# Optimization experiments

Hardware: AMD Instinct MI355X
Metric: run time of the kernel (lower is better)

Reference implementation:

```python
import jax, jax.numpy as jnp
import numpy as np

TOP_K = 2
LORA_SCALE = 32.0 / 16.0  # alpha / rank


def setup_inputs() -> dict:
    key = jax.random.key(0)
    ks = jax.random.split(key, 11)
    N, D, F, E, R = 1024, 2048, 5632, 8, 16
    s = lambda k, shape, fan: jax.random.normal(k, shape, jnp.float32) / np.sqrt(fan)
    return {
        "x": jax.random.normal(ks[0], (N, D), jnp.float32),
        "gate_w": s(ks[1], (E, D), D),
        "W1": s(ks[2], (F, D), D),
        "W3": s(ks[3], (F, D), D),
        "W2": s(ks[4], (D, F), F),
        "A1": s(ks[5], (E, R, D), D),
        "B1": s(ks[6], (F, R), R)[None].repeat(E, 0) * 0.0 + s(ks[6], (E, F, R), R),
        "A3": s(ks[7], (E, R, D), D),
        "B3": s(ks[8], (E, F, R), R),
        "A2": s(ks[9], (E, R, F), F),
        "B2": s(ks[10], (E, D, R), R),
    }


def reference(x, gate_w, W1, W3, W2, A1, B1, A3, B3, A2, B2):
    # --- router: softmax over experts, top-k, renormalized combine weights ---
    logits = x @ gate_w.T                                   # [N, E]
    probs = jax.nn.softmax(logits, axis=-1)
    topw, topi = jax.lax.top_k(probs, TOP_K)                # [N, K]
    topw = topw / jnp.sum(topw, axis=-1, keepdims=True)
    E = gate_w.shape[0]
    w = jnp.sum(jax.nn.one_hot(topi, E, dtype=x.dtype) * topw[..., None], axis=1)  # [N, E]

    # --- experts: shared base weights + per-expert LoRA (fused SwiGLU) ---
    base1 = x @ W1.T                                        # [N, F]
    base3 = x @ W3.T                                        # [N, F]
    l1 = jnp.einsum("nd,erd->ner", x, A1)                   # rank-R bottleneck
    l3 = jnp.einsum("nd,erd->ner", x, A3)
    h1 = base1[:, None, :] + LORA_SCALE * jnp.einsum("ner,efr->nef", l1, B1)  # [N, E, F]
    h3 = base3[:, None, :] + LORA_SCALE * jnp.einsum("ner,efr->nef", l3, B3)
    s = jax.nn.silu(h1) * h3                                # [N, E, F]

    # down-projection: shared W2 applied to the routed mixture, plus per-expert LoRA
    s_mix = jnp.einsum("ne,nef->nf", w, s)                  # [N, F]
    out = s_mix @ W2.T                                      # [N, D]
    l2 = jnp.einsum("nef,erf->ner", s, A2) * (w[:, :, None] * LORA_SCALE)
    out = out + jnp.einsum("ner,edr->nd", l2, B2)           # [N, D]
    return out, logits
```

## Files before the change

### kernel.cpp

```cpp
#include <hip/hip_runtime.h>

typedef unsigned int u32;
typedef unsigned short u16;

#define N_TOK 1024
#define D_DIM 2048
#define F_DIM 5632
#define E_NUM 8
#define R_DIM 16
#define LSCALE 2.0f
#define FT 256
#define NT (F_DIM / FT)
#define TC 8
#define BN13 11520

typedef __bf16 bf16x8 __attribute__((ext_vector_type(8)));
typedef float f32x4 __attribute__((ext_vector_type(4)));
typedef u16 u16x8 __attribute__((ext_vector_type(8)));

__device__ inline u16 f2bf(float f) {
    u32 u = __builtin_bit_cast(u32, f);
    u32 r = (u + 0x7fffu + ((u >> 16) & 1u)) >> 16;
    return (u16)r;
}
__device__ inline float bf2f(u16 h) {
    u32 u = ((u32)h) << 16;
    return __builtin_bit_cast(float, u);
}

__global__ __launch_bounds__(256) void cvt_f32_bf16(const float* __restrict__ src,
                                                    u16* __restrict__ dst, int n4) {
    int i = blockIdx.x * 256 + threadIdx.x;
    if (i >= n4) return;
    float4 v = ((const float4*)src)[i];
    union { u16 h[4]; ushort4 u4; } o;
    o.h[0] = f2bf(v.x); o.h[1] = f2bf(v.y); o.h[2] = f2bf(v.z); o.h[3] = f2bf(v.w);
    ((ushort4*)dst)[i] = o.u4;
}

__global__ __launch_bounds__(256) void a2_transpose(const float* __restrict__ A2,
                                                    u16* __restrict__ A2t) {
    int e = blockIdx.y;
    int f = blockIdx.x * 256 + threadIdx.x;
    u16 row[16];
#pragma unroll
    for (int r = 0; r < 16; ++r)
        row[r] = f2bf(A2[((size_t)e * R_DIM + r) * F_DIM + f]);
    u16* dst = A2t + ((size_t)e * F_DIM + f) * 16;
#pragma unroll
    for (int q = 0; q < 2; ++q)
        ((ulonglong2*)dst)[q] = ((ulonglong2*)row)[q];
}

__global__ __launch_bounds__(256) void router_kernel(const float* __restrict__ x,
                                                     const float* __restrict__ gw,
                                                     float* __restrict__ logits,
                                                     int* __restrict__ ridx,
                                                     float* __restrict__ rw) {
    int n = blockIdx.x;
    int tid = threadIdx.x;
    float part[E_NUM];
#pragma unroll
    for (int e = 0; e < E_NUM; ++e) part[e] = 0.f;
    const float* xr = x + (size_t)n * D_DIM;
    for (int d = tid; d < D_DIM; d += 256) {
        float xv = xr[d];
#pragma unroll
        for (int e = 0; e < E_NUM; ++e) part[e] += xv * gw[e * D_DIM + d];
    }
    __shared__ float sh[E_NUM][256];
#pragma unroll
    for (int e = 0; e < E_NUM; ++e) sh[e][tid] = part[e];
    __syncthreads();
    for (int off = 128; off > 0; off >>= 1) {
        if (tid < off) {
#pragma unroll
            for (int e = 0; e < E_NUM; ++e) sh[e][tid] += sh[e][tid + off];
        }
        __syncthreads();
    }
    if (tid == 0) {
        float lg[E_NUM], p[E_NUM];
        float mx = -1e30f;
        for (int e = 0; e < E_NUM; ++e) {
            lg[e] = sh[e][0];
            logits[n * E_NUM + e] = lg[e];
            if (lg[e] > mx) mx = lg[e];
        }
        float s = 0.f;
        for (int e = 0; e < E_NUM; ++e) { p[e] = expf(lg[e] - mx); s += p[e]; }
        for (int e = 0; e < E_NUM; ++e) p[e] /= s;
        int i1 = 0;
        for (int e = 1; e < E_NUM; ++e) if (p[e] > p[i1]) i1 = e;
        int i2 = (i1 == 0) ? 1 : 0;
        for (int e = 0; e < E_NUM; ++e) if (e != i1 && p[e] > p[i2]) i2 = e;
        float t = p[i1] + p[i2];
        ridx[n * 2] = i1; ridx[n * 2 + 1] = i2;
        rw[n * 2] = p[i1] / t; rw[n * 2 + 1] = p[i2] / t;
    }
}

__global__ __launch_bounds__(64) void zero_counts(int* counts) {
    if (threadIdx.x < E_NUM) counts[threadIdx.x] = 0;
}
__global__ __launch_bounds__(256) void build_lists(const int* __restrict__ ridx,
                                                   int* __restrict__ counts,
                                                   u32* __restrict__ lists) {
    int n = blockIdx.x * 256 + threadIdx.x;
    if (n >= N_TOK) return;
#pragma unroll
    for (int k = 0; k < 2; ++k) {
        int e = ridx[n * 2 + k];
        int slot = atomicAdd(&counts[e], 1);
        lists[e * N_TOK + slot] = (u32)n | ((u32)k << 16);
    }
}

__global__ __launch_bounds__(256) void gemm_bf16_bt(const u16* __restrict__ A,
                                                    const u16* __restrict__ B,
                                                    float* __restrict__ C,
                                                    int M, int N, int K, int out_bf16) {
    __shared__ __align__(16) u16 sA[128 * 64];
    __shared__ __align__(16) u16 sB[128 * 64];
    const int tid = threadIdx.x;
    const int lane = tid & 63;
    const int wave = tid >> 6;
    const int quad = lane >> 4;
    const int l16 = lane & 15;
    const int wm = (wave & 1) * 64;
    const int wn = (wave >> 1) * 64;
    const int bm0 = blockIdx.x * 128;
    const int bn0 = blockIdx.y * 128;

    f32x4 zero = {0.f, 0.f, 0.f, 0.f};
    f32x4 acc[4][4];
#pragma unroll
    for (int i = 0; i < 4; ++i)
#pragma unroll
        for (int j = 0; j < 4; ++j) acc[i][j] = zero;

    for (int k0 = 0; k0 < K; k0 += 64) {
#pragma unroll
        for (int i = 0; i < 4; ++i) {
            int c = i * 256 + tid;
            int r = c >> 3;
            int c8 = (c & 7) << 3;
            const u16* ga = A + (size_t)(bm0 + r) * K + k0 + c8;
            const u16* gb = B + (size_t)(bn0 + r) * K + k0 + c8;
            __builtin_amdgcn_global_load_lds((const __attribute__((address_space(1))) u32*)ga,
                                             (__attribute__((address_space(3))) u32*)(sA + c * 8),
                                             16, 0, 0);
            __builtin_amdgcn_global_load_lds((const __attribute__((address_space(1))) u32*)gb,
                                             (__attribute__((address_space(3))) u32*)(sB + c * 8),
                                             16, 0, 0);
        }
        __syncthreads();
#pragma unroll
        for (int ks = 0; ks < 2; ++ks) {
            bf16x8 af[4], bfv[4];
#pragma unroll
            for (int mi = 0; mi < 4; ++mi)
                af[mi] = *(const bf16x8*)(sA + (wm + mi * 16 + l16) * 64 + ks * 32 + quad * 8);
#pragma unroll
            for (int ni = 0; ni < 4; ++ni)
                bfv[ni] = *(const bf16x8*)(sB + (wn + ni * 16 + l16) * 64 + ks * 32 + quad * 8);
#pragma unroll
            for (int mi = 0; mi < 4; ++mi)
#pragma unroll
                for (int ni = 0; ni < 4; ++ni)
                    acc[mi][ni] = __builtin_amdgcn_mfma_f32_16x16x32_bf16(af[mi], bfv[ni],
                                                                          acc[mi][ni], 0, 0, 0);
        }
        __syncthreads();
    }

#pragma unroll
    for (int mi = 0; mi < 4; ++mi)
#pragma unroll
        for (int ni = 0; ni < 4; ++ni) {
            int col = bn0 + wn + ni * 16 + l16;
#pragma unroll
            for (int i = 0; i < 4; ++i) {
                int row = bm0 + wm + mi * 16 + quad * 4 + i;
                if (out_bf16) {
                    ((u16*)C)[(size_t)row * N + col] = f2bf(acc[mi][ni][i]);
                } else {
                    C[(size_t)row * N + col] = acc[mi][ni][i];
                }
            }
        }
}

__global__ __launch_bounds__(256) void gemm_bt_splitk(const u16* __restrict__ A,
                                                      const u16* __restrict__ B,
                                                      float* __restrict__ C,
                                                      int M, int N, int K, int ksplit) {
    __shared__ __align__(16) u16 sA[128 * 64];
    __shared__ __align__(16) u16 sB[128 * 64];
    const int tid = threadIdx.x;
    const int lane = tid & 63;
    const int wave = tid >> 6;
    const int quad = lane >> 4;
    const int l16 = lane & 15;
    const int wm = (wave & 1) * 64;
    const int wn = (wave >> 1) * 64;
    const int bm0 = blockIdx.x * 128;
    const int bn0 = blockIdx.y * 128;
    const int kb = blockIdx.z * ksplit;
    const int ke = kb + ksplit;

    f32x4 zero = {0.f, 0.f, 0.f, 0.f};
    f32x4 acc[4][4];
#pragma unroll
    for (int i = 0; i < 4; ++i)
#pragma unroll
        for (int j = 0; j < 4; ++j) acc[i][j] = zero;

    for (int k0 = kb; k0 < ke; k0 += 64) {
#pragma unroll
        for (int i = 0; i < 4; ++i) {
            int c = i * 256 + tid;
            int r = c >> 3;
            int c8 = (c & 7) << 3;
            const u16* ga = A + (size_t)(bm0 + r) * K + k0 + c8;
            const u16* gb = B + (size_t)(bn0 + r) * K + k0 + c8;
            __builtin_amdgcn_global_load_lds((const __attribute__((address_space(1))) u32*)ga,
                                             (__attribute__((address_space(3))) u32*)(sA + c * 8),
                                             16, 0, 0);
            __builtin_amdgcn_global_load_lds((const __attribute__((address_space(1))) u32*)gb,
                                             (__attribute__((address_space(3))) u32*)(sB + c * 8),
                                             16, 0, 0);
        }
        __syncthreads();
#pragma unroll
        for (int ks = 0; ks < 2; ++ks) {
            bf16x8 af[4], bfv[4];
#pragma unroll
            for (int mi = 0; mi < 4; ++mi)
                af[mi] = *(const bf16x8*)(sA + (wm + mi * 16 + l16) * 64 + ks * 32 + quad * 8);
#pragma unroll
            for (int ni = 0; ni < 4; ++ni)
                bfv[ni] = *(const bf16x8*)(sB + (wn + ni * 16 + l16) * 64 + ks * 32 + quad * 8);
#pragma unroll
            for (int mi = 0; mi < 4; ++mi)
#pragma unroll
                for (int ni = 0; ni < 4; ++ni)
                    acc[mi][ni] = __builtin_amdgcn_mfma_f32_16x16x32_bf16(af[mi], bfv[ni],
                                                                          acc[mi][ni], 0, 0, 0);
        }
        __syncthreads();
    }

#pragma unroll
    for (int mi = 0; mi < 4; ++mi)
#pragma unroll
        for (int ni = 0; ni < 4; ++ni) {
            int col = bn0 + wn + ni * 16 + l16;
#pragma unroll
            for (int i = 0; i < 4; ++i) {
                int row = bm0 + wm + mi * 16 + quad * 4 + i;
                unsafeAtomicAdd(&C[(size_t)row * N + col], acc[mi][ni][i]);
            }
        }
}

__global__ __launch_bounds__(256) void act_v2b(const u16* __restrict__ base13,
                                               const u16* __restrict__ B1b,
                                               const u16* __restrict__ B3b,
                                               const u32* __restrict__ lists,
                                               const int* __restrict__ counts,
                                               const float* __restrict__ rw,
                                               u16* __restrict__ sbuf) {
    const int ft = blockIdx.x;
    const int e  = blockIdx.y;
    const int z  = blockIdx.z;
    const int tid = threadIdx.x;
    const int lane = tid & 63;
    const int wave = tid >> 6;
    const int f_lane = ft * FT + lane * 4;

    u16x8 w1c[8], w3c[8];
    {
        const u16* p1 = B1b + ((size_t)e * F_DIM + f_lane) * 16;
        const u16* p3 = B3b + ((size_t)e * F_DIM + f_lane) * 16;
#pragma unroll
        for (int c = 0; c < 8; ++c) {
            w1c[c] = *(const u16x8*)(p1 + c * 8);
            w3c[c] = *(const u16x8*)(p3 + c * 8);
        }
    }

    const int T = counts[e];
    for (int i = z * 4 + wave; i < T; i += TC * 4) {
        u32 ent = lists[e * N_TOK + i];
        int n = (int)(ent & 0xFFFFu);
        int k = (int)(ent >> 16);
        float wt = rw[n * 2 + k];

        float la1[16], la3[16];
        {
            const u16x8* pl1 = (const u16x8*)(base13 + (size_t)n * BN13 + 11264 + e * 16);
            const u16x8* pl3 = (const u16x8*)(base13 + (size_t)n * BN13 + 11392 + e * 16);
#pragma unroll
            for (int h = 0; h < 2; ++h) {
                u16x8 t1 = pl1[h], t3 = pl3[h];
#pragma unroll
                for (int q = 0; q < 8; ++q) {
                    la1[h * 8 + q] = LSCALE * bf2f(t1[q]);
                    la3[h * 8 + q] = LSCALE * bf2f(t3[q]);
                }
            }
        }

        ushort4 b1u = *(const ushort4*)(base13 + (size_t)n * BN13 + f_lane);
        ushort4 b3u = *(const ushort4*)(base13 + (size_t)n * BN13 + 5632 + f_lane);
        const u16* b1p = (const u16*)&b1u;
        const u16* b3p = (const u16*)&b3u;

        u16 sv[4];
#pragma unroll
        for (int j = 0; j < 4; ++j) {
            float h1 = bf2f(b1p[j]);
            float h3 = bf2f(b3p[j]);
#pragma unroll
            for (int q = 0; q < 8; ++q) {
                h1 += la1[q] * bf2f(w1c[2 * j][q]);
                h3 += la3[q] * bf2f(w3c[2 * j][q]);
            }
#pragma unroll
            for (int q = 0; q < 8; ++q) {
                h1 += la1[8 + q] * bf2f(w1c[2 * j + 1][q]);
                h3 += la3[8 + q] * bf2f(w3c[2 * j + 1][q]);
            }
            float sg = h1 / (1.f + __expf(-h1));
            sv[j] = f2bf(wt * sg * h3);
        }
        *(ushort4*)(sbuf + ((size_t)k * N_TOK + n) * F_DIM + f_lane) = *(ushort4*)sv;
    }
}

__global__ __launch_bounds__(256) void combine_kernel(const u16* __restrict__ sbuf,
                                                      u16* __restrict__ smix) {
    size_t i = ((size_t)blockIdx.x * 256 + threadIdx.x) * 8;
    u16x8 a = *(const u16x8*)(sbuf + i);
    u16x8 b = *(const u16x8*)(sbuf + (size_t)N_TOK * F_DIM + i);
    u16x8 o;
#pragma unroll
    for (int q = 0; q < 8; ++q) o[q] = f2bf(bf2f(a[q]) + bf2f(b[q]));
    *(u16x8*)(smix + i) = o;
}

__global__ __launch_bounds__(256) void lora_down_v3(const u16* __restrict__ sbuf,
                                                    const u16* __restrict__ A2t,
                                                    const int* __restrict__ ridx,
                                                    const float* __restrict__ B2,
                                                    float* __restrict__ out) {
    const int n = blockIdx.x, tid = threadIdx.x;
    __shared__ float part[2][32][16];
    __shared__ float fin[2][16];
    __shared__ int se[2];
    if (tid < 2) se[tid] = ridx[n * 2 + tid];
    __syncthreads();

    {
        const int k = tid >> 7;
        const int tt = tid & 127;
        const int rq = tt & 3;
        const int fc = tt >> 2;
        const int e = se[k];
        const u16* srow = sbuf + ((size_t)k * N_TOK + n) * F_DIM + fc * 176;
        const u16* arow = A2t + ((size_t)e * F_DIM + fc * 176) * 16 + rq * 4;
        float acc0 = 0.f, acc1 = 0.f, acc2 = 0.f, acc3 = 0.f;
#pragma unroll 4
        for (int f = 0; f < 176; ++f) {
            float sv = bf2f(srow[f]);
            ushort4 wr = *(const ushort4*)(arow + (size_t)f * 16);
            acc0 += sv * bf2f(wr.x);
            acc1 += sv * bf2f(wr.y);
            acc2 += sv * bf2f(wr.z);
            acc3 += sv * bf2f(wr.w);
        }
        part[k][fc][rq * 4 + 0] = acc0;
        part[k][fc][rq * 4 + 1] = acc1;
        part[k][fc][rq * 4 + 2] = acc2;
        part[k][fc][rq * 4 + 3] = acc3;
    }
    __syncthreads();
    if (tid < 32) {
        int k = tid >> 4, r = tid & 15;
        float s = 0.f;
#pragma unroll
        for (int fc = 0; fc < 32; ++fc) s += part[k][fc][r];
        fin[k][r] = LSCALE * s;
    }
    __syncthreads();

    float a0[16], a1v[16];
#pragma unroll
    for (int r = 0; r < 16; ++r) { a0[r] = fin[0][r]; a1v[r] = fin[1][r]; }
    const float* B2a = B2 + (size_t)se[0] * D_DIM * R_DIM;
    const float* B2b = B2 + (size_t)se[1] * D_DIM * R_DIM;
    float* orow = out + (size_t)n * D_DIM;
    for (int d = tid; d < D_DIM; d += 256) {
        const float4* pa = (const float4*)(B2a + (size_t)d * 16);
        const float4* pb = (const float4*)(B2b + (size_t)d * 16);
        float acc = 0.f;
#pragma unroll
        for (int q = 0; q < 4; ++q) {
            float4 va = pa[q];
            acc += a0[q * 4] * va.x + a0[q * 4 + 1] * va.y +
                   a0[q * 4 + 2] * va.z + a0[q * 4 + 3] * va.w;
            float4 vb = pb[q];
            acc += a1v[q * 4] * vb.x + a1v[q * 4 + 1] * vb.y +
                   a1v[q * 4 + 2] * vb.z + a1v[q * 4 + 3] * vb.w;
        }
        orow[d] = acc;
    }
}

extern "C" void kernel_launch(void* const* d_in, const int* in_sizes, int n_in,
                              void* d_out, int out_size, void* d_ws, size_t ws_size,
                              hipStream_t stream) {
    const float* x  = (const float*)d_in[0];
    const float* gw = (const float*)d_in[1];
    const float* W1 = (const float*)d_in[2];
    const float* W3 = (const float*)d_in[3];
    const float* W2 = (const float*)d_in[4];
    const float* A1 = (const float*)d_in[5];
    const float* B1 = (const float*)d_in[6];
    const float* A3 = (const float*)d_in[7];
    const float* B3 = (const float*)d_in[8];
    const float* A2 = (const float*)d_in[9];
    const float* B2 = (const float*)d_in[10];
    float* out = (float*)d_out;
    float* logits = out + (size_t)N_TOK * D_DIM;

    char* ws = (char*)d_ws;
    size_t off = 0;
    auto alloc = [&](size_t bytes) { char* p = ws + off; off += (bytes + 255) & ~(size_t)255; return p; };
    u16*   xb    = (u16*)alloc((size_t)N_TOK * D_DIM * 2);
    u16*   W13b  = (u16*)alloc((size_t)BN13 * D_DIM * 2);
    u16*   W2b   = (u16*)alloc((size_t)D_DIM * F_DIM * 2);
    u16*   base13= (u16*)alloc((size_t)N_TOK * BN13 * 2);
    int*   ridx  = (int*)alloc((size_t)N_TOK * 2 * 4);
    float* rwt   = (float*)alloc((size_t)N_TOK * 2 * 4);
    u16*   B1b   = (u16*)alloc((size_t)E_NUM * F_DIM * R_DIM * 2);
    u16*   B3b   = (u16*)alloc((size_t)E_NUM * F_DIM * R_DIM * 2);
    u16*   A2t   = (u16*)alloc((size_t)E_NUM * F_DIM * R_DIM * 2);
    int*   counts= (int*)alloc(64);
    u32*   lists = (u32*)alloc((size_t)E_NUM * N_TOK * 4);
    u16*   sbuf  = (u16*)alloc((size_t)2 * N_TOK * F_DIM * 2);
    u16*   smixb = (u16*)alloc((size_t)N_TOK * F_DIM * 2);
    (void)ws_size; (void)in_sizes; (void)n_in; (void)out_size;

    auto cvt = [&](const float* s, u16* d, size_t cnt) {
        int n4 = (int)(cnt / 4);
        cvt_f32_bf16<<<(n4 + 255) / 256, 256, 0, stream>>>(s, d, n4);
    };
    cvt(x,  xb,  (size_t)N_TOK * D_DIM);
    cvt(W1, W13b, (size_t)F_DIM * D_DIM);
    cvt(W3, W13b + (size_t)F_DIM * D_DIM, (size_t)F_DIM * D_DIM);
    cvt(A1, W13b + (size_t)2 * F_DIM * D_DIM, (size_t)128 * D_DIM);
    cvt(A3, W13b + (size_t)2 * F_DIM * D_DIM + (size_t)128 * D_DIM, (size_t)128 * D_DIM);
    cvt(W2, W2b, (size_t)D_DIM * F_DIM);
    cvt(B1, B1b, (size_t)E_NUM * F_DIM * R_DIM);
    cvt(B3, B3b, (size_t)E_NUM * F_DIM * R_DIM);
    a2_transpose<<<dim3(F_DIM / 256, E_NUM), 256, 0, stream>>>(A2, A2t);

    router_kernel<<<N_TOK, 256, 0, stream>>>(x, gw, logits, ridx, rwt);
    zero_counts<<<1, 64, 0, stream>>>(counts);
    build_lists<<<N_TOK / 256, 256, 0, stream>>>(ridx, counts, lists);

    gemm_bf16_bt<<<dim3(N_TOK / 128, BN13 / 128), 256, 0, stream>>>(xb, W13b, (float*)base13,
                                                                    N_TOK, BN13, D_DIM, 1);

    act_v2b<<<dim3(NT, E_NUM, TC), 256, 0, stream>>>(base13, B1b, B3b,
                                                     lists, counts, rwt, sbuf);

    combine_kernel<<<(N_TOK * F_DIM / 8) / 256, 256, 0, stream>>>(sbuf, smixb);

    lora_down_v3<<<N_TOK, 256, 0, stream>>>(sbuf, A2t, ridx, B2, out);

    gemm_bt_splitk<<<dim3(N_TOK / 128, D_DIM / 128, 4), 256, 0, stream>>>(smixb, W2b, out,
                                                                          N_TOK, D_DIM, F_DIM,
                                                                          F_DIM / 4);
}
```

Before: 466.3 us.

## Use 256x256 double-buffered GEMM with XCD-aware tile mapping; fuse conversions

Replaces both 128x128 GEMM kernels with one 256x256-tile, 512-thread kernel. It double-buffers LDS so the next K-slice loads while MFMAs run, and remaps block IDs so neighbouring tiles land on the same XCD for L2 reuse. The down-projection keeps split-K with atomics, now 8 slices of 704. The eight separate f32-to-bf16 conversion launches are merged into one kernel to cut launch overhead. Larger tiles mean fewer blocks (180 and 256), which risks lower occupancy and higher register pressure; the 64 KB per buffer in LDS may also limit residency.

```diff
diff --git a/kernel.cpp b/kernel.cpp
--- a/kernel.cpp
+++ b/kernel.cpp
@@ -28,14 +28,35 @@
     return __builtin_bit_cast(float, u);
 }
 
-__global__ __launch_bounds__(256) void cvt_f32_bf16(const float* __restrict__ src,
-                                                    u16* __restrict__ dst, int n4) {
+__global__ __launch_bounds__(256) void cvt_all(const float* __restrict__ x,
+                                               const float* __restrict__ W1,
+                                               const float* __restrict__ W3,
+                                               const float* __restrict__ A1,
+                                               const float* __restrict__ A3,
+                                               const float* __restrict__ W2,
+                                               const float* __restrict__ B1,
+                                               const float* __restrict__ B3,
+                                               u16* __restrict__ xb,
+                                               u16* __restrict__ w13,
+                                               u16* __restrict__ w2b,
+                                               u16* __restrict__ b1b,
+                                               u16* __restrict__ b3b) {
     int i = blockIdx.x * 256 + threadIdx.x;
-    if (i >= n4) return;
-    float4 v = ((const float4*)src)[i];
+    const float* src;
+    u16* dst;
+    int off;
+    if (i < 524288)       { src = x;  dst = xb;             off = i; }
+    else if (i < 3407872) { src = W1; dst = w13;            off = i - 524288; }
+    else if (i < 6291456) { src = W3; dst = w13 + 11534336; off = i - 3407872; }
+    else if (i < 6356992) { src = A1; dst = w13 + 23068672; off = i - 6291456; }
+    else if (i < 6422528) { src = A3; dst = w13 + 23330816; off = i - 6356992; }
+    else if (i < 9306112) { src = W2; dst = w2b;            off = i - 6422528; }
+    else if (i < 9486336) { src = B1; dst = b1b;            off = i - 9306112; }
+    else                  { src = B3; dst = b3b;            off = i - 9486336; }
+    float4 v = ((const float4*)src)[off];
     union { u16 h[4]; ushort4 u4; } o;
     o.h[0] = f2bf(v.x); o.h[1] = f2bf(v.y); o.h[2] = f2bf(v.z); o.h[3] = f2bf(v.w);
-    ((ushort4*)dst)[i] = o.u4;
+    ((ushort4*)dst)[off] = o.u4;
 }
 
 __global__ __launch_bounds__(256) void a2_transpose(const float* __restrict__ A2,
@@ -116,150 +137,103 @@
     }
 }
 
-__global__ __launch_bounds__(256) void gemm_bf16_bt(const u16* __restrict__ A,
-                                                    const u16* __restrict__ B,
-                                                    float* __restrict__ C,
-                                                    int M, int N, int K, int out_bf16) {
-    __shared__ __align__(16) u16 sA[128 * 64];
-    __shared__ __align__(16) u16 sB[128 * 64];
+__global__ __launch_bounds__(512, 2) void gemm256(const u16* __restrict__ A,
+                                                  const u16* __restrict__ B,
+                                                  float* __restrict__ C,
+                                                  int N, int K, int kslice,
+                                                  int mode, int ntm, int ntn) {
+    __shared__ __align__(16) u16 sA[2][256 * 64];
+    __shared__ __align__(16) u16 sB[2][256 * 64];
+
+    const int nb = gridDim.x;
+    const int f = blockIdx.x;
+    const int q = nb >> 3, r = nb & 7;
+    const int xcd = f & 7, lo = f >> 3;
+    const int wg = (xcd < r ? xcd * (q + 1) : r * (q + 1) + (xcd - r) * q) + lo;
+
+    const int mt = wg % ntm;
+    const int t2 = wg / ntm;
+    const int nt = t2 % ntn;
+    const int zt = t2 / ntn;
+
+    const int bm0 = mt * 256;
+    const int bn0 = nt * 256;
+    const int kb = zt * kslice;
+
     const int tid = threadIdx.x;
     const int lane = tid & 63;
     const int wave = tid >> 6;
     const int quad = lane >> 4;
     const int l16 = lane & 15;
-    const int wm = (wave & 1) * 64;
-    const int wn = (wave >> 1) * 64;
-    const int bm0 = blockIdx.x * 128;
-    const int bn0 = blockIdx.y * 128;
+    const int wm = (wave >> 2) * 128;
+    const int wn = (wave & 3) * 64;
 
     f32x4 zero = {0.f, 0.f, 0.f, 0.f};
-    f32x4 acc[4][4];
-#pragma unroll
-    for (int i = 0; i < 4; ++i)
+    f32x4 acc[8][4];
+#pragma unroll
+    for (int i = 0; i < 8; ++i)
 #pragma unroll
         for (int j = 0; j < 4; ++j) acc[i][j] = zero;
 
-    for (int k0 = 0; k0 < K; k0 += 64) {
+    auto stage = [&](int buf, int k0) {
 #pragma unroll
         for (int i = 0; i < 4; ++i) {
-            int c = i * 256 + tid;
-            int r = c >> 3;
+            int c = i * 512 + tid;
+            int rr = c >> 3;
             int c8 = (c & 7) << 3;
-            const u16* ga = A + (size_t)(bm0 + r) * K + k0 + c8;
-            const u16* gb = B + (size_t)(bn0 + r) * K + k0 + c8;
+            const u16* ga = A + (size_t)(bm0 + rr) * K + k0 + c8;
+            const u16* gb = B + (size_t)(bn0 + rr) * K + k0 + c8;
             __builtin_amdgcn_global_load_lds((const __attribute__((address_space(1))) u32*)ga,
-                                             (__attribute__((address_space(3))) u32*)(sA + c * 8),
+                                             (__attribute__((address_space(3))) u32*)(&sA[buf][c * 8]),
                                              16, 0, 0);
             __builtin_amdgcn_global_load_lds((const __attribute__((address_space(1))) u32*)gb,
-                                             (__attribute__((address_space(3))) u32*)(sB + c * 8),
+                                             (__attribute__((address_space(3))) u32*)(&sB[buf][c * 8]),
                                              16, 0, 0);
         }
-        __syncthreads();
+    };
+
+    const int nk = kslice >> 6;
+    int cur = 0;
+    stage(0, kb);
+    __syncthreads();
+
+    for (int kt = 0; kt < nk; ++kt) {
+        if (kt + 1 < nk) stage(cur ^ 1, kb + (kt + 1) * 64);
 #pragma unroll
         for (int ks = 0; ks < 2; ++ks) {
-            bf16x8 af[4], bfv[4];
-#pragma unroll
-            for (int mi = 0; mi < 4; ++mi)
-                af[mi] = *(const bf16x8*)(sA + (wm + mi * 16 + l16) * 64 + ks * 32 + quad * 8);
+            bf16x8 af[8], bfv[4];
+#pragma unroll
+            for (int mi = 0; mi < 8; ++mi)
+                af[mi] = *(const bf16x8*)(&sA[cur][(wm + mi * 16 + l16) * 64 + ks * 32 + quad * 8]);
 #pragma unroll
             for (int ni = 0; ni < 4; ++ni)
-                bfv[ni] = *(const bf16x8*)(sB + (wn + ni * 16 + l16) * 64 + ks * 32 + quad * 8);
-#pragma unroll
-            for (int mi = 0; mi < 4; ++mi)
+                bfv[ni] = *(const bf16x8*)(&sB[cur][(wn + ni * 16 + l16) * 64 + ks * 32 + quad * 8]);
+#pragma unroll
+            for (int mi = 0; mi < 8; ++mi)
 #pragma unroll
                 for (int ni = 0; ni < 4; ++ni)
                     acc[mi][ni] = __builtin_amdgcn_mfma_f32_16x16x32_bf16(af[mi], bfv[ni],
                                                                           acc[mi][ni], 0, 0, 0);
         }
         __syncthreads();
-    }
-
-#pragma unroll
-    for (int mi = 0; mi < 4; ++mi)
+        cur ^= 1;
+    }
+
+#pragma unroll
+    for (int mi = 0; mi < 8; ++mi)
 #pragma unroll
         for (int ni = 0; ni < 4; ++ni) {
             int col = bn0 + wn + ni * 16 + l16;
 #pragma unroll
             for (int i = 0; i < 4; ++i) {
                 int row = bm0 + wm + mi * 16 + quad * 4 + i;
-                if (out_bf16) {
+                if (mode == 1) {
                     ((u16*)C)[(size_t)row * N + col] = f2bf(acc[mi][ni][i]);
+                } else if (mode == 2) {
+                    unsafeAtomicAdd(&C[(size_t)row * N + col], acc[mi][ni][i]);
                 } else {
                     C[(size_t)row * N + col] = acc[mi][ni][i];
                 }
-            }
-        }
-}
-
-__global__ __launch_bounds__(256) void gemm_bt_splitk(const u16* __restrict__ A,
-                                                      const u16* __restrict__ B,
-                                                      float* __restrict__ C,
-                                                      int M, int N, int K, int ksplit) {
-    __shared__ __align__(16) u16 sA[128 * 64];
-    __shared__ __align__(16) u16 sB[128 * 64];
-    const int tid = threadIdx.x;
-    const int lane = tid & 63;
-    const int wave = tid >> 6;
-    const int quad = lane >> 4;
-    const int l16 = lane & 15;
-    const int wm = (wave & 1) * 64;
-    const int wn = (wave >> 1) * 64;
-    const int bm0 = blockIdx.x * 128;
-    const int bn0 = blockIdx.y * 128;
-    const int kb = blockIdx.z * ksplit;
-    const int ke = kb + ksplit;
-
-    f32x4 zero = {0.f, 0.f, 0.f, 0.f};
-    f32x4 acc[4][4];
-#pragma unroll
-    for (int i = 0; i < 4; ++i)
-#pragma unroll
-        for (int j = 0; j < 4; ++j) acc[i][j] = zero;
-
-    for (int k0 = kb; k0 < ke; k0 += 64) {
-#pragma unroll
-        for (int i = 0; i < 4; ++i) {
-            int c = i * 256 + tid;
-            int r = c >> 3;
-            int c8 = (c & 7) << 3;
-            const u16* ga = A + (size_t)(bm0 + r) * K + k0 + c8;
-            const u16* gb = B + (size_t)(bn0 + r) * K + k0 + c8;
-            __builtin_amdgcn_global_load_lds((const __attribute__((address_space(1))) u32*)ga,
-                                             (__attribute__((address_space(3))) u32*)(sA + c * 8),
-                                             16, 0, 0);
-            __builtin_amdgcn_global_load_lds((const __attribute__((address_space(1))) u32*)gb,
-                                             (__attribute__((address_space(3))) u32*)(sB + c * 8),
-                                             16, 0, 0);
-        }
-        __syncthreads();
-#pragma unroll
-        for (int ks = 0; ks < 2; ++ks) {
-            bf16x8 af[4], bfv[4];
-#pragma unroll
-            for (int mi = 0; mi < 4; ++mi)
-                af[mi] = *(const bf16x8*)(sA + (wm + mi * 16 + l16) * 64 + ks * 32 + quad * 8);
-#pragma unroll
-            for (int ni = 0; ni < 4; ++ni)
-                bfv[ni] = *(const bf16x8*)(sB + (wn + ni * 16 + l16) * 64 + ks * 32 + quad * 8);
-#pragma unroll
-            for (int mi = 0; mi < 4; ++mi)
-#pragma unroll
-                for (int ni = 0; ni < 4; ++ni)
-                    acc[mi][ni] = __builtin_amdgcn_mfma_f32_16x16x32_bf16(af[mi], bfv[ni],
-                                                                          acc[mi][ni], 0, 0, 0);
-        }
-        __syncthreads();
-    }
-
-#pragma unroll
-    for (int mi = 0; mi < 4; ++mi)
-#pragma unroll
-        for (int ni = 0; ni < 4; ++ni) {
-            int col = bn0 + wn + ni * 16 + l16;
-#pragma unroll
-            for (int i = 0; i < 4; ++i) {
-                int row = bm0 + wm + mi * 16 + quad * 4 + i;
-                unsafeAtomicAdd(&C[(size_t)row * N + col], acc[mi][ni][i]);
             }
         }
 }
@@ -305,9 +279,9 @@
             for (int h = 0; h < 2; ++h) {
                 u16x8 t1 = pl1[h], t3 = pl3[h];
 #pragma unroll
-                for (int q = 0; q < 8; ++q) {
-                    la1[h * 8 + q] = LSCALE * bf2f(t1[q]);
-                    la3[h * 8 + q] = LSCALE * bf2f(t3[q]);
+                for (int qq = 0; qq < 8; ++qq) {
+                    la1[h * 8 + qq] = LSCALE * bf2f(t1[qq]);
+                    la3[h * 8 + qq] = LSCALE * bf2f(t3[qq]);
                 }
             }
         }
@@ -323,14 +297,14 @@
             float h1 = bf2f(b1p[j]);
             float h3 = bf2f(b3p[j]);
 #pragma unroll
-            for (int q = 0; q < 8; ++q) {
-                h1 += la1[q] * bf2f(w1c[2 * j][q]);
-                h3 += la3[q] * bf2f(w3c[2 * j][q]);
+            for (int qq = 0; qq < 8; ++qq) {
+                h1 += la1[qq] * bf2f(w1c[2 * j][qq]);
+                h3 += la3[qq] * bf2f(w3c[2 * j][qq]);
             }
 #pragma unroll
-            for (int q = 0; q < 8; ++q) {
-                h1 += la1[8 + q] * bf2f(w1c[2 * j + 1][q]);
-                h3 += la3[8 + q] * bf2f(w3c[2 * j + 1][q]);
+            for (int qq = 0; qq < 8; ++qq) {
+                h1 += la1[8 + qq] * bf2f(w1c[2 * j + 1][qq]);
+                h3 += la3[8 + qq] * bf2f(w3c[2 * j + 1][qq]);
             }
             float sg = h1 / (1.f + __expf(-h1));
             sv[j] = f2bf(wt * sg * h3);
@@ -453,26 +427,16 @@
     u16*   smixb = (u16*)alloc((size_t)N_TOK * F_DIM * 2);
     (void)ws_size; (void)in_sizes; (void)n_in; (void)out_size;
 
-    auto cvt = [&](const float* s, u16* d, size_t cnt) {
-        int n4 = (int)(cnt / 4);
-        cvt_f32_bf16<<<(n4 + 255) / 256, 256, 0, stream>>>(s, d, n4);
-    };
-    cvt(x,  xb,  (size_t)N_TOK * D_DIM);
-    cvt(W1, W13b, (size_t)F_DIM * D_DIM);
-    cvt(W3, W13b + (size_t)F_DIM * D_DIM, (size_t)F_DIM * D_DIM);
-    cvt(A1, W13b + (size_t)2 * F_DIM * D_DIM, (size_t)128 * D_DIM);
-    cvt(A3, W13b + (size_t)2 * F_DIM * D_DIM + (size_t)128 * D_DIM, (size_t)128 * D_DIM);
-    cvt(W2, W2b, (size_t)D_DIM * F_DIM);
-    cvt(B1, B1b, (size_t)E_NUM * F_DIM * R_DIM);
-    cvt(B3, B3b, (size_t)E_NUM * F_DIM * R_DIM);
+    cvt_all<<<37760, 256, 0, stream>>>(x, W1, W3, A1, A3, W2, B1, B3,
+                                       xb, W13b, W2b, B1b, B3b);
     a2_transpose<<<dim3(F_DIM / 256, E_NUM), 256, 0, stream>>>(A2, A2t);
 
     router_kernel<<<N_TOK, 256, 0, stream>>>(x, gw, logits, ridx, rwt);
     zero_counts<<<1, 64, 0, stream>>>(counts);
     build_lists<<<N_TOK / 256, 256, 0, stream>>>(ridx, counts, lists);
 
-    gemm_bf16_bt<<<dim3(N_TOK / 128, BN13 / 128), 256, 0, stream>>>(xb, W13b, (float*)base13,
-                                                                    N_TOK, BN13, D_DIM, 1);
+    gemm256<<<180, 512, 0, stream>>>(xb, W13b, (float*)base13,
+                                     BN13, D_DIM, D_DIM, 1, 4, 45);
 
     act_v2b<<<dim3(NT, E_NUM, TC), 256, 0, stream>>>(base13, B1b, B3b,
                                                      lists, counts, rwt, sbuf);
@@ -481,7 +445,6 @@
 
     lora_down_v3<<<N_TOK, 256, 0, stream>>>(sbuf, A2t, ridx, B2, out);
 
-    gemm_bt_splitk<<<dim3(N_TOK / 128, D_DIM / 128, 4), 256, 0, stream>>>(smixb, W2b, out,
-                                                                          N_TOK, D_DIM, F_DIM,
-                                                                          F_DIM / 4);
-}
+    gemm256<<<256, 512, 0, stream>>>(smixb, W2b, out,
+                                     D_DIM, F_DIM, 704, 2, 4, 8);
+}
```

Measured after the change: 464.5 us. No clear change (-0.4%).
